# Kernel optimization log

Measured on AMD Instinct MI355X. Metric: run time of the kernel, lower is better.

The kernel has to match this reference:

```python
import jax, jax.numpy as jnp
import numpy as np

COMMITMENT_COST = 0.25
KLD_SCALE = 1.0


def setup_inputs() -> dict:
    key = jax.random.key(0)
    k1, k2 = jax.random.split(key)
    z = jax.random.normal(k1, (8, 4096, 512), dtype=jnp.float32)
    embed_w = jax.random.normal(k2, (1024, 512), dtype=jnp.float32)
    return {"z": z, "embed_w": embed_w}


def reference(z, embed_w):
    bsz, s, d = z.shape
    flat = z.reshape(-1, d)  # [N, d]
    dist = (
        jnp.sum(flat * flat, axis=1, keepdims=True)
        - 2.0 * flat @ embed_w.T
        + jnp.sum(embed_w * embed_w, axis=1)[None, :]
    )
    ind = jnp.argmin(dist, axis=1).reshape(bsz, s)  # (-dist).max == dist.min
    z_q = embed_w[ind]  # codebook gather [bsz, s, d]
    sg = jax.lax.stop_gradient
    diff = COMMITMENT_COST * ((sg(z_q) - z) ** 2 + (z_q - sg(z)) ** 2)
    diff = diff * KLD_SCALE
    z_q = z + sg(z_q - z)  # straight-through estimator
    return z_q, diff, ind
```

## Files before the change

### kernel.cpp

```cpp
#include <hip/hip_runtime.h>
#include <math.h>


#define D_DIM   512
#define K_CODES 1024
#define N_TOK   32768

#define BM 128
#define BN 128
#define NKT 16

typedef __attribute__((ext_vector_type(8))) short bf16x8;
typedef __attribute__((ext_vector_type(4))) float f32x4;

__device__ __forceinline__ unsigned short bf16_rne(float f) {
    unsigned int u = __float_as_uint(f);
    return (unsigned short)((u + 0x7FFFu + ((u >> 16) & 1u)) >> 16);
}
__device__ __forceinline__ float bf16_to_f32(unsigned short b) {
    return __uint_as_float(((unsigned int)b) << 16);
}

#define GLOAD16(gp, lp)                                                        \
    __builtin_amdgcn_global_load_lds(                                          \
        (const __attribute__((address_space(1))) void*)(gp),                   \
        (__attribute__((address_space(3))) void*)(lp), 16, 0, 0)

__global__ __launch_bounds__(256) void vq_zsplit(const float* __restrict__ z,
                                                 unsigned short* __restrict__ zhi,
                                                 unsigned short* __restrict__ zlo) {
    const int tid = blockIdx.x * 256 + threadIdx.x;
    const float4* z4 = (const float4*)z;
    ushort4* h4 = (ushort4*)zhi;
    ushort4* l4 = (ushort4*)zlo;
#pragma unroll
    for (int g = 0; g < 8; ++g) {
        const size_t i = (size_t)g * 524288 + tid;
        float4 v = z4[i];
        float f[4] = {v.x, v.y, v.z, v.w};
        unsigned short hb[4], lb[4];
#pragma unroll
        for (int j = 0; j < 4; ++j) {
            hb[j] = bf16_rne(f[j]);
            lb[j] = bf16_rne(f[j] - bf16_to_f32(hb[j]));
        }
        h4[i] = make_ushort4(hb[0], hb[1], hb[2], hb[3]);
        l4[i] = make_ushort4(lb[0], lb[1], lb[2], lb[3]);
    }
}

__global__ __launch_bounds__(256) void vq_prep(const float* __restrict__ ew,
                                               unsigned short* __restrict__ ehi,
                                               unsigned short* __restrict__ elo,
                                               float* __restrict__ e2) {
    const int wv = threadIdx.x >> 6, lane = threadIdx.x & 63;
    const int code = blockIdx.x * 4 + wv;
    const float* row = ew + (size_t)code * D_DIM;
    float s = 0.0f;
#pragma unroll
    for (int h = 0; h < 2; ++h) {
        const int c = h * 256 + lane * 4;
        float4 v = *(const float4*)(row + c);
        float f[4] = {v.x, v.y, v.z, v.w};
        unsigned short hb[4], lb[4];
#pragma unroll
        for (int j = 0; j < 4; ++j) {
            s = fmaf(f[j], f[j], s);
            hb[j] = bf16_rne(f[j]);
            lb[j] = bf16_rne(f[j] - bf16_to_f32(hb[j]));
        }
        *(ushort4*)(ehi + (size_t)code * D_DIM + c) = make_ushort4(hb[0], hb[1], hb[2], hb[3]);
        *(ushort4*)(elo + (size_t)code * D_DIM + c) = make_ushort4(lb[0], lb[1], lb[2], lb[3]);
    }
#pragma unroll
    for (int off = 32; off > 0; off >>= 1) s += __shfl_xor(s, off, 64);
    if (lane == 0) e2[code] = s;
}

__global__ __launch_bounds__(256, 3) void vq_gemm(
    const unsigned short* __restrict__ zhi, const unsigned short* __restrict__ zlo,
    const unsigned short* __restrict__ ehi, const unsigned short* __restrict__ elo,
    const float* __restrict__ e2, float* __restrict__ pv, float* __restrict__ pif) {
    __shared__ __align__(16) unsigned short lds[16384];
    const int AHI = 0, ALO = 4096, BHI = 8192, BLO = 12288;

    const int t = threadIdx.x, lane = t & 63, wv = t >> 6;
    const int b  = blockIdx.x;
    const int wg = (b & 7) * 256 + (b >> 3);
    const int mtile = wg >> 3, ntile = wg & 7;
    const int row0 = mtile * BM;
    const int c0g  = ntile * BN;

    const int idx0 = (wv * 2 + 0) * 64 + lane;
    const int idx1 = (wv * 2 + 1) * 64 + lane;
    const int c_0 = idx0 >> 7, r_0 = idx0 & 127;
    const int c_1 = idx1 >> 7, r_1 = idx1 & 127;
    const size_t zo0 = (size_t)(row0 + r_0) * D_DIM + c_0 * 8;
    const size_t zo1 = (size_t)(row0 + r_1) * D_DIM + c_1 * 8;
    const size_t eo0 = (size_t)(c0g + r_0) * D_DIM + c_0 * 8;
    const size_t eo1 = (size_t)(c0g + r_1) * D_DIM + c_1 * 8;
    const int l0 = (wv * 2 + 0) * 512;
    const int l1 = (wv * 2 + 1) * 512;

    const int wr = wv >> 1, wc = wv & 1;
    const int lm = lane & 15, lk = lane >> 4;

    f32x4 acc[4][4];
    const f32x4 zero4 = {0.f, 0.f, 0.f, 0.f};
#pragma unroll
    for (int i = 0; i < 4; ++i)
#pragma unroll
        for (int j = 0; j < 4; ++j) acc[i][j] = zero4;

    for (int kt = 0; kt < NKT; ++kt) {
        const int ko = kt * 32;
        GLOAD16(zhi + zo0 + ko, &lds[AHI + l0]);
        GLOAD16(zhi + zo1 + ko, &lds[AHI + l1]);
        GLOAD16(zlo + zo0 + ko, &lds[ALO + l0]);
        GLOAD16(zlo + zo1 + ko, &lds[ALO + l1]);
        GLOAD16(ehi + eo0 + ko, &lds[BHI + l0]);
        GLOAD16(ehi + eo1 + ko, &lds[BHI + l1]);
        GLOAD16(elo + eo0 + ko, &lds[BLO + l0]);
        GLOAD16(elo + eo1 + ko, &lds[BLO + l1]);
        __syncthreads();

        bf16x8 ah[4], al[4], bh[4], bl[4];
#pragma unroll
        for (int mi = 0; mi < 4; ++mi) {
            const int s = (lk * 128 + wr * 64 + mi * 16 + lm) * 8;
            ah[mi] = *(const bf16x8*)&lds[AHI + s];
            al[mi] = *(const bf16x8*)&lds[ALO + s];
        }
#pragma unroll
        for (int nj = 0; nj < 4; ++nj) {
            const int s = (lk * 128 + wc * 64 + nj * 16 + lm) * 8;
            bh[nj] = *(const bf16x8*)&lds[BHI + s];
            bl[nj] = *(const bf16x8*)&lds[BLO + s];
        }
#pragma unroll
        for (int mi = 0; mi < 4; ++mi)
#pragma unroll
            for (int nj = 0; nj < 4; ++nj)
                acc[mi][nj] = __builtin_amdgcn_mfma_f32_16x16x32_bf16(
                    ah[mi], bh[nj], acc[mi][nj], 0, 0, 0);
#pragma unroll
        for (int mi = 0; mi < 4; ++mi)
#pragma unroll
            for (int nj = 0; nj < 4; ++nj)
                acc[mi][nj] = __builtin_amdgcn_mfma_f32_16x16x32_bf16(
                    ah[mi], bl[nj], acc[mi][nj], 0, 0, 0);
#pragma unroll
        for (int mi = 0; mi < 4; ++mi)
#pragma unroll
            for (int nj = 0; nj < 4; ++nj)
                acc[mi][nj] = __builtin_amdgcn_mfma_f32_16x16x32_bf16(
                    al[mi], bh[nj], acc[mi][nj], 0, 0, 0);
        __syncthreads();
    }

    float best[16], bidx[16];
#pragma unroll
    for (int i = 0; i < 16; ++i) { best[i] = INFINITY; bidx[i] = 0.f; }
#pragma unroll
    for (int nj = 0; nj < 4; ++nj) {
        const int cloc = wc * 64 + nj * 16 + lm;
        const float e2v = e2[c0g + cloc];
#pragma unroll
        for (int mi = 0; mi < 4; ++mi)
#pragma unroll
            for (int r = 0; r < 4; ++r) {
                const float sc = fmaf(-2.0f, acc[mi][nj][r], e2v);
                const int bi = mi * 4 + r;
                if (sc < best[bi]) { best[bi] = sc; bidx[bi] = (float)(c0g + cloc); }
            }
    }
#pragma unroll
    for (int off = 1; off < 16; off <<= 1) {
#pragma unroll
        for (int bi = 0; bi < 16; ++bi) {
            float v2 = __shfl_xor(best[bi], off, 64);
            float i2 = __shfl_xor(bidx[bi], off, 64);
            if (v2 < best[bi] || (v2 == best[bi] && i2 < bidx[bi])) {
                best[bi] = v2; bidx[bi] = i2;
            }
        }
    }
    __syncthreads();
    float* sv = (float*)lds;
    float* si = sv + 256;
    if (lm == 0) {
#pragma unroll
        for (int mi = 0; mi < 4; ++mi)
#pragma unroll
            for (int r = 0; r < 4; ++r) {
                const int rl = wr * 64 + mi * 16 + lk * 4 + r;
                sv[wc * 128 + rl] = best[mi * 4 + r];
                si[wc * 128 + rl] = bidx[mi * 4 + r];
            }
    }
    __syncthreads();
    if (t < 128) {
        float v0 = sv[t], i0 = si[t];
        float v1 = sv[128 + t], i1 = si[128 + t];
        if (v1 < v0 || (v1 == v0 && i1 < i0)) { v0 = v1; i0 = i1; }
        pv [(size_t)ntile * N_TOK + row0 + t] = v0;
        pif[(size_t)ntile * N_TOK + row0 + t] = i0;
    }
}

__global__ __launch_bounds__(256) void vq_reduce(const float* __restrict__ pv,
                                                 const float* __restrict__ pif,
                                                 float* __restrict__ indf) {
    const int row = blockIdx.x * 256 + threadIdx.x;
    float v = pv[row], ix = pif[row];
#pragma unroll
    for (int nb = 1; nb < 8; ++nb) {
        float v2 = pv[(size_t)nb * N_TOK + row];
        float i2 = pif[(size_t)nb * N_TOK + row];
        if (v2 < v || (v2 == v && i2 < ix)) { v = v2; ix = i2; }
    }
    indf[row] = ix;
}

__global__ __launch_bounds__(256) void vq_out_kernel(
    const float* __restrict__ z, const float* __restrict__ ew,
    const float* __restrict__ indf, float* __restrict__ zq,
    float* __restrict__ diff) {
    const int w    = threadIdx.x >> 6;
    const int lane = threadIdx.x & 63;
    const int row  = blockIdx.x * 4 + w;
    const int c    = (int)indf[row];

    const float4* z4 = (const float4*)&z[(size_t)row * D_DIM];
    const float4* e4 = (const float4*)&ew[(size_t)c * D_DIM];
    float4* q4 = (float4*)&zq[(size_t)row * D_DIM];
    float4* d4 = (float4*)&diff[(size_t)row * D_DIM];

#pragma unroll
    for (int v = 0; v < 2; ++v) {
        const int i = v * 64 + lane;
        const float4 zv = z4[i];
        const float4 ev = e4[i];
        float4 qv, dv;
        float ax = ev.x - zv.x, ay = ev.y - zv.y, az = ev.z - zv.z, aw = ev.w - zv.w;
        qv.x = zv.x + ax; qv.y = zv.y + ay; qv.z = zv.z + az; qv.w = zv.w + aw;
        dv.x = 0.5f * (ax * ax); dv.y = 0.5f * (ay * ay);
        dv.z = 0.5f * (az * az); dv.w = 0.5f * (aw * aw);
        q4[i] = qv;
        d4[i] = dv;
    }
}

extern "C" void kernel_launch(void* const* d_in, const int* in_sizes, int n_in,
                              void* d_out, int out_size, void* d_ws, size_t ws_size,
                              hipStream_t stream) {
    const float* z  = (const float*)d_in[0];
    const float* ew = (const float*)d_in[1];
    float* out  = (float*)d_out;
    float* zq   = out;
    float* diff = out + (size_t)N_TOK * D_DIM;
    float* indf = out + (size_t)2 * N_TOK * D_DIM;

    char* s0 = (char*)d_out;
    unsigned short* ehi = (unsigned short*)(s0);
    unsigned short* elo = (unsigned short*)(s0 + (1u << 20));
    float* e2  = (float*)(s0 + (2u << 20));
    float* pv  = (float*)(s0 + (2u << 20) + 4096);
    float* pif = (float*)(s0 + (3u << 20) + 4096);
    unsigned short* zhi = (unsigned short*)diff;
    unsigned short* zlo = zhi + (size_t)N_TOK * D_DIM;

    hipLaunchKernelGGL(vq_zsplit, dim3(2048),       dim3(256), 0, stream, z, zhi, zlo);
    hipLaunchKernelGGL(vq_prep,   dim3(K_CODES / 4), dim3(256), 0, stream, ew, ehi, elo, e2);
    hipLaunchKernelGGL(vq_gemm,   dim3(2048),       dim3(256), 0, stream,
                       zhi, zlo, ehi, elo, e2, pv, pif);
    hipLaunchKernelGGL(vq_reduce, dim3(N_TOK / 256), dim3(256), 0, stream, pv, pif, indf);
    hipLaunchKernelGGL(vq_out_kernel, dim3(N_TOK / 4), dim3(256), 0, stream,
                       z, ew, indf, zq, diff);
}
```

Measured before the change: 196.9 us.

## Double-buffer GEMM LDS tiles and fuse argmin reduction into output kernel

The GEMM main loop now uses two LDS buffers: the global-to-LDS loads for the next k-tile are issued before computing on the current one, so memory latency can overlap MFMA work. LDS use doubles and the occupancy hint drops from 3 to 2 blocks per CU. The separate reduce kernel is removed, and each wave of the output kernel now reduces the 8 partial argmins with shuffles before gathering. This saves one launch and one round trip through memory. Partial results move into the workspace buffer.

```diff
diff --git a/kernel.cpp b/kernel.cpp
--- a/kernel.cpp
+++ b/kernel.cpp
@@ -77,11 +77,11 @@
     if (lane == 0) e2[code] = s;
 }
 
-__global__ __launch_bounds__(256, 3) void vq_gemm(
+__global__ __launch_bounds__(256, 2) void vq_gemm(
     const unsigned short* __restrict__ zhi, const unsigned short* __restrict__ zlo,
     const unsigned short* __restrict__ ehi, const unsigned short* __restrict__ elo,
     const float* __restrict__ e2, float* __restrict__ pv, float* __restrict__ pif) {
-    __shared__ __align__(16) unsigned short lds[16384];
+    __shared__ __align__(16) unsigned short lds[32768];
     const int AHI = 0, ALO = 4096, BHI = 8192, BLO = 12288;
 
     const int t = threadIdx.x, lane = t & 63, wv = t >> 6;
@@ -112,30 +112,38 @@
 #pragma unroll
         for (int j = 0; j < 4; ++j) acc[i][j] = zero4;
 
+    auto stage = [&](int kt, int bufo) {
+        const int ko = kt * 32;
+        GLOAD16(zhi + zo0 + ko, &lds[bufo + AHI + l0]);
+        GLOAD16(zhi + zo1 + ko, &lds[bufo + AHI + l1]);
+        GLOAD16(zlo + zo0 + ko, &lds[bufo + ALO + l0]);
+        GLOAD16(zlo + zo1 + ko, &lds[bufo + ALO + l1]);
+        GLOAD16(ehi + eo0 + ko, &lds[bufo + BHI + l0]);
+        GLOAD16(ehi + eo1 + ko, &lds[bufo + BHI + l1]);
+        GLOAD16(elo + eo0 + ko, &lds[bufo + BLO + l0]);
+        GLOAD16(elo + eo1 + ko, &lds[bufo + BLO + l1]);
+    };
+
+    stage(0, 0);
+    __syncthreads();
+
+    int cur = 0;
     for (int kt = 0; kt < NKT; ++kt) {
-        const int ko = kt * 32;
-        GLOAD16(zhi + zo0 + ko, &lds[AHI + l0]);
-        GLOAD16(zhi + zo1 + ko, &lds[AHI + l1]);
-        GLOAD16(zlo + zo0 + ko, &lds[ALO + l0]);
-        GLOAD16(zlo + zo1 + ko, &lds[ALO + l1]);
-        GLOAD16(ehi + eo0 + ko, &lds[BHI + l0]);
-        GLOAD16(ehi + eo1 + ko, &lds[BHI + l1]);
-        GLOAD16(elo + eo0 + ko, &lds[BLO + l0]);
-        GLOAD16(elo + eo1 + ko, &lds[BLO + l1]);
-        __syncthreads();
+        const int bufo = cur * 16384;
+        if (kt + 1 < NKT) stage(kt + 1, (cur ^ 1) * 16384);
 
         bf16x8 ah[4], al[4], bh[4], bl[4];
 #pragma unroll
         for (int mi = 0; mi < 4; ++mi) {
             const int s = (lk * 128 + wr * 64 + mi * 16 + lm) * 8;
-            ah[mi] = *(const bf16x8*)&lds[AHI + s];
-            al[mi] = *(const bf16x8*)&lds[ALO + s];
+            ah[mi] = *(const bf16x8*)&lds[bufo + AHI + s];
+            al[mi] = *(const bf16x8*)&lds[bufo + ALO + s];
         }
 #pragma unroll
         for (int nj = 0; nj < 4; ++nj) {
             const int s = (lk * 128 + wc * 64 + nj * 16 + lm) * 8;
-            bh[nj] = *(const bf16x8*)&lds[BHI + s];
-            bl[nj] = *(const bf16x8*)&lds[BLO + s];
+            bh[nj] = *(const bf16x8*)&lds[bufo + BHI + s];
+            bl[nj] = *(const bf16x8*)&lds[bufo + BLO + s];
         }
 #pragma unroll
         for (int mi = 0; mi < 4; ++mi)
@@ -155,7 +163,9 @@
             for (int nj = 0; nj < 4; ++nj)
                 acc[mi][nj] = __builtin_amdgcn_mfma_f32_16x16x32_bf16(
                     al[mi], bh[nj], acc[mi][nj], 0, 0, 0);
+
         __syncthreads();
+        cur ^= 1;
     }
 
     float best[16], bidx[16];
@@ -208,28 +218,28 @@
     }
 }
 
-__global__ __launch_bounds__(256) void vq_reduce(const float* __restrict__ pv,
-                                                 const float* __restrict__ pif,
-                                                 float* __restrict__ indf) {
-    const int row = blockIdx.x * 256 + threadIdx.x;
-    float v = pv[row], ix = pif[row];
-#pragma unroll
-    for (int nb = 1; nb < 8; ++nb) {
-        float v2 = pv[(size_t)nb * N_TOK + row];
-        float i2 = pif[(size_t)nb * N_TOK + row];
-        if (v2 < v || (v2 == v && i2 < ix)) { v = v2; ix = i2; }
-    }
-    indf[row] = ix;
-}
-
 __global__ __launch_bounds__(256) void vq_out_kernel(
     const float* __restrict__ z, const float* __restrict__ ew,
-    const float* __restrict__ indf, float* __restrict__ zq,
-    float* __restrict__ diff) {
+    const float* __restrict__ pv, const float* __restrict__ pif,
+    float* __restrict__ indf, float* __restrict__ zq, float* __restrict__ diff) {
     const int w    = threadIdx.x >> 6;
     const int lane = threadIdx.x & 63;
     const int row  = blockIdx.x * 4 + w;
-    const int c    = (int)indf[row];
+
+    float v = INFINITY, ix = 0.f;
+    if (lane < 8) {
+        v  = pv [(size_t)lane * N_TOK + row];
+        ix = pif[(size_t)lane * N_TOK + row];
+    }
+#pragma unroll
+    for (int off = 1; off < 8; off <<= 1) {
+        float v2 = __shfl_xor(v, off, 64);
+        float i2 = __shfl_xor(ix, off, 64);
+        if (v2 < v || (v2 == v && i2 < ix)) { v = v2; ix = i2; }
+    }
+    const float ixb = __shfl(ix, 0, 64);
+    const int c = (int)ixb;
+    if (lane == 0) indf[row] = ixb;
 
     const float4* z4 = (const float4*)&z[(size_t)row * D_DIM];
     const float4* e4 = (const float4*)&ew[(size_t)c * D_DIM];
@@ -237,8 +247,8 @@
     float4* d4 = (float4*)&diff[(size_t)row * D_DIM];
 
 #pragma unroll
-    for (int v = 0; v < 2; ++v) {
-        const int i = v * 64 + lane;
+    for (int vv = 0; vv < 2; ++vv) {
+        const int i = vv * 64 + lane;
         const float4 zv = z4[i];
         const float4 ev = e4[i];
         float4 qv, dv;
@@ -265,16 +275,15 @@
     unsigned short* ehi = (unsigned short*)(s0);
     unsigned short* elo = (unsigned short*)(s0 + (1u << 20));
     float* e2  = (float*)(s0 + (2u << 20));
-    float* pv  = (float*)(s0 + (2u << 20) + 4096);
-    float* pif = (float*)(s0 + (3u << 20) + 4096);
     unsigned short* zhi = (unsigned short*)diff;
     unsigned short* zlo = zhi + (size_t)N_TOK * D_DIM;
-
-    hipLaunchKernelGGL(vq_zsplit, dim3(2048),       dim3(256), 0, stream, z, zhi, zlo);
+    float* pv  = (float*)d_ws;
+    float* pif = (float*)d_ws + (size_t)8 * N_TOK;
+
+    hipLaunchKernelGGL(vq_zsplit, dim3(2048),        dim3(256), 0, stream, z, zhi, zlo);
     hipLaunchKernelGGL(vq_prep,   dim3(K_CODES / 4), dim3(256), 0, stream, ew, ehi, elo, e2);
-    hipLaunchKernelGGL(vq_gemm,   dim3(2048),       dim3(256), 0, stream,
+    hipLaunchKernelGGL(vq_gemm,   dim3(2048),        dim3(256), 0, stream,
                        zhi, zlo, ehi, elo, e2, pv, pif);
-    hipLaunchKernelGGL(vq_reduce, dim3(N_TOK / 256), dim3(256), 0, stream, pv, pif, indf);
     hipLaunchKernelGGL(vq_out_kernel, dim3(N_TOK / 4), dim3(256), 0, stream,
-                       z, ew, indf, zq, diff);
-}
+                       z, ew, pv, pif, indf, zq, diff);
+}
```

New measurement: 209.8 us. 1.07x slower.
